# Kernel optimization log

Measured on AMD Instinct MI355X. Metric: run time of the kernel, lower is better.

Reference implementation:

```python
import jax, jax.numpy as jnp
import numpy as np

C = jnp.complex64
NQ = 4  # qubits per register (module-level `qubits` constant)

_CNOT = jnp.array([[1,0,0,0],[0,1,0,0],[0,0,0,1],[0,0,1,0]], dtype=C)
_X = jnp.array([[0,1],[1,0]], dtype=C)

def _RZ(t):
    e = jnp.exp((-0.5j) * t.astype(C))
    z = jnp.zeros((), C)
    return jnp.stack([jnp.stack([e, z]), jnp.stack([z, jnp.conj(e)])])

def _RX(t):
    c = jnp.cos(0.5 * t).astype(C)
    s = (-1j) * jnp.sin(0.5 * t).astype(C)
    return jnp.stack([jnp.stack([c, s]), jnp.stack([s, c])])

def _CRX(t):
    return jnp.eye(4, dtype=C).at[2:, 2:].set(_RX(t))

def _IXX(t):
    c = jnp.cos(0.5 * t).astype(C)
    s = (-1j) * jnp.sin(0.5 * t).astype(C)
    return c * jnp.eye(4, dtype=C) + s * jnp.fliplr(jnp.eye(4, dtype=C))

def _ap1(psi, U, w):
    psi = jnp.moveaxis(psi, w, 0)
    psi = jnp.tensordot(U, psi, axes=([1], [0]))
    return jnp.moveaxis(psi, 0, w)

def _ap2(psi, U, w1, w2):
    psi = jnp.moveaxis(psi, (w1, w2), (0, 1))
    shp = psi.shape
    psi = (U @ psi.reshape(4, -1)).reshape(shp)
    return jnp.moveaxis(psi, (0, 1), (w1, w2))

def _expZ(psi, w):
    p = psi.real ** 2 + psi.imag ** 2
    p = jnp.moveaxis(p, w, 0).reshape(2, -1).sum(axis=1)
    return p[0] - p[1]

def _expX(psi, w):
    return jnp.real(jnp.vdot(psi, _ap1(psi, _X, w)))

def _init_state(n):
    return jnp.zeros((2,) * n, C).at[(0,) * n].set(1.0 + 0.0j)

def _rot_layer(psi, rot, offset, start):
    for i in range(NQ):
        idx = start + 3 * i
        w = offset + i
        psi = _ap1(psi, _RZ(rot[idx]), w)
        psi = _ap1(psi, _RX(rot[idx + 1]), w)
        psi = _ap1(psi, _RZ(rot[idx + 2]), w)
    return psi

def _two_ring(psi, rot, crx, offset):
    # depth == 2 (24 rot params): one rot layer before entanglers, one after.
    psi = _rot_layer(psi, rot, offset, 0)
    for i in range(NQ):
        psi = _ap2(psi, _CRX(crx[i]), offset + i, offset + (i + 1) % NQ)
    for i in range(NQ):  # len(crx)==2*NQ -> IsingXX ring
        psi = _ap2(psi, _IXX(crx[NQ + i]), offset + i, offset + (i + 1) % NQ)
    psi = _rot_layer(psi, rot, offset, 3 * NQ)
    return psi

def _score_circuit(xq, xk, wq_rot, wq_crx, wk_rot, wk_crx, wc_rot, wc_crx, wc_crx2):
    psi = _init_state(2 * NQ)
    for i in range(NQ):  # AngleEmbedding (default rotation='X')
        psi = _ap1(psi, _RX(xq[i]), i)
    psi = _two_ring(psi, wq_rot, wq_crx, 0)
    for i in range(NQ):
        psi = _ap1(psi, _RX(xk[i]), NQ + i)
    psi = _two_ring(psi, wk_rot, wk_crx, NQ)
    for i in range(NQ):
        psi = _ap2(psi, _CRX(wc_crx[i]), i, i + NQ)
        psi = _ap2(psi, _CRX(wc_crx[i + NQ]), i + NQ, i)
    for i in range(NQ):
        psi = _ap2(psi, _CRX(wc_crx2[i]), i, (i + 1) % NQ + NQ)
    for i in range(NQ):
        psi = _ap2(psi, _CRX(wc_crx2[i + NQ]), i + NQ, (i + 1) % NQ)
    for i in range(NQ):
        psi = _ap2(psi, _CNOT, i, i + NQ)
        psi = _ap2(psi, _CNOT, i + NQ, i)
    psi = _rot_layer(psi, wc_rot, 0, 0)
    z = jnp.stack([_expZ(psi, w) for w in range(NQ)])
    x = jnp.stack([_expX(psi, w) for w in range(NQ)])
    return jnp.concatenate([z, x])

def _value_circuit(xv, amp, wv_rot, wv_crx, gates):
    psi = _init_state(NQ)
    for i in range(NQ):
        psi = _ap1(psi, _RX(xv[i]), i)
    psi = _two_ring(psi, wv_rot, wv_crx, 0)
    for i in range(NQ):
        psi = _ap1(psi, _RX(jnp.tanh(amp[i]) * gates[i]), i)
    for i in range(NQ):
        psi = _ap2(psi, _CNOT, i, (i + 1) % NQ)
    z = jnp.stack([_expZ(psi, w) for w in range(NQ)])
    x = jnp.stack([_expX(psi, w) for w in range(NQ)])
    return jnp.concatenate([z, x])

def setup_inputs() -> dict:
    key = jax.random.key(0)
    ks = jax.random.split(key, 16)
    B, IN = 4096, 96
    hp = np.pi / 2
    return {
        'x_text': jax.random.normal(ks[0], (B, IN), jnp.float32),
        'x_image': jax.random.normal(ks[1], (B, IN), jnp.float32),
        'W_text': jax.random.normal(ks[2], (NQ, IN), jnp.float32) * 0.1,
        'b_text': jnp.zeros((NQ,), jnp.float32),
        'W_image': jax.random.normal(ks[3], (NQ, IN), jnp.float32) * 0.1,
        'b_image': jnp.zeros((NQ,), jnp.float32),
        'weights_q_rot': jax.random.uniform(ks[4], (6 * NQ,), jnp.float32, -hp, hp),
        'weights_q_crx': jax.random.normal(ks[5], (2 * NQ,), jnp.float32) * 0.1,
        'weights_k_rot': jax.random.uniform(ks[6], (6 * NQ,), jnp.float32, -hp, hp),
        'weights_k_crx': jax.random.normal(ks[7], (2 * NQ,), jnp.float32) * 0.1,
        'weights_v_rot': jax.random.uniform(ks[8], (6 * NQ,), jnp.float32, -hp, hp),
        'weights_v_crx': jax.random.normal(ks[9], (2 * NQ,), jnp.float32) * 0.1,
        'weights_cross_rot': jax.random.uniform(ks[10], (3 * NQ,), jnp.float32, -hp, hp),
        'weights_cross_crx': jax.random.normal(ks[11], (2 * NQ,), jnp.float32) * 0.1,
        'weights_cross_crx2': jax.random.normal(ks[12], (2 * NQ,), jnp.float32) * 0.1,
        'score_gates': jnp.full((NQ,), np.pi, jnp.float32),
    }

def reference(x_text, x_image, W_text, b_text, W_image, b_image,
              weights_q_rot, weights_q_crx, weights_k_rot, weights_k_crx,
              weights_v_rot, weights_v_crx, weights_cross_rot,
              weights_cross_crx, weights_cross_crx2, score_gates):
    # anneal alpha = 1.0 and all QAFConfig flags True -> effective params = raw params
    xq = x_text @ W_text.T + b_text   # [B, 4]
    xk = x_image @ W_image.T + b_image
    score = jax.vmap(lambda a, b: _score_circuit(
        a, b, weights_q_rot, weights_q_crx, weights_k_rot, weights_k_crx,
        weights_cross_rot, weights_cross_crx, weights_cross_crx2))(xq, xk)  # [B, 8]
    amp = jnp.sqrt(score[:, :NQ] ** 2 + score[:, NQ:] ** 2)  # [B, 4]
    out = jax.vmap(lambda v, a: _value_circuit(
        v, a, weights_v_rot, weights_v_crx, score_gates))(xk, amp)  # [B, 8]
    return out.astype(jnp.float32)
```

## Files before the change

kernel.cpp:

```cpp
#include <hip/hip_runtime.h>
#include <math.h>

#define DEV __device__ __forceinline__

template<int M>
DEV float lxor(float x) {
    const int i = __builtin_bit_cast(int, x);
    int r;
    if constexpr (M == 1)      r = __builtin_amdgcn_update_dpp(i, i, 0xB1, 0xF, 0xF, false);
    else if constexpr (M == 2) r = __builtin_amdgcn_update_dpp(i, i, 0x4E, 0xF, 0xF, false);
    else if constexpr (M == 3) r = __builtin_amdgcn_update_dpp(i, i, 0x1B, 0xF, 0xF, false);
    else if constexpr (M == 8) r = __builtin_amdgcn_update_dpp(i, i, 0x128, 0xF, 0xF, false);
    else                       r = __builtin_amdgcn_ds_swizzle(i, (M << 10) | 0x1F);
    return __builtin_bit_cast(float, r);
}
template<int M> DEV float2 lxor2(float2 v) {
    return make_float2(lxor<M>(v.x), lxor<M>(v.y));
}
DEV float red16(float x) {
    x += lxor<8>(x); x += lxor<4>(x); x += lxor<2>(x); x += lxor<1>(x);
    return x;
}
DEV float red32(float x) {
    x += lxor<16>(x);
    return red16(x);
}

template<int LM>
DEV void sgate(float2& v, int l16, float2 u00, float2 u01) {
    const bool hi = (l16 & LM) != 0;
    const float e00x = u00.x, e00y = hi ? -u00.y : u00.y;
    const float e01x = hi ? -u01.x : u01.x, e01y = u01.y;
    const float2 p = lxor2<LM>(v);
    v = make_float2(e00x*v.x - e00y*v.y + e01x*p.x - e01y*p.y,
                    e00x*v.y + e00y*v.x + e01x*p.y + e01y*p.x);
}
template<int LM>
DEV void sgate4(float2& v, int l16, float4 g) {
    sgate<LM>(v, l16, make_float2(g.x, g.y), make_float2(g.z, g.w));
}
template<int CL, int LM>
DEV void scrx(float2& v, int l16, float2 cs) {
    const bool hi = (l16 & CL) != 0;
    const float c = hi ? cs.x : 1.f, sn = hi ? cs.y : 0.f;
    const float2 p = lxor2<LM>(v);
    v = make_float2(c*v.x + sn*p.y, c*v.y - sn*p.x);
}
template<int LM2>
DEV void sixx(float2& v, float2 cs) {
    const float2 p = lxor2<LM2>(v);
    v = make_float2(cs.x*v.x + cs.y*p.y, cs.x*v.y - cs.y*p.x);
}
template<int LM>
DEV void srx(float2& v, float c, float sn) {
    const float2 p = lxor2<LM>(v);
    v = make_float2(c*v.x + sn*p.y, c*v.y - sn*p.x);
}
template<int CL, int LM>
DEV void scnot(float2& v, int l16) {
    const float2 p = lxor2<LM>(v);
    const bool hi = (l16 & CL) != 0;
    v = hi ? p : v;
}

template<int CM, int LM>
DEV void fcrx_rl(float2 (&s)[8], float2 cs) {
#pragma unroll
    for (int r = 0; r < 8; r++) {
        if (!(r & CM)) continue;
        const float2 p = lxor2<LM>(s[r]);
        const float2 a = s[r];
        s[r] = make_float2(cs.x*a.x + cs.y*p.y, cs.x*a.y - cs.y*p.x);
    }
}
template<int CL, int RM>
DEV void fcrx_lr(float2 (&s)[8], int l32, float2 cs) {
    const bool hi = (l32 & CL) != 0;
    const float c = hi ? cs.x : 1.f, sn = hi ? cs.y : 0.f;
#pragma unroll
    for (int r = 0; r < 8; r++) {
        if (r & RM) continue;
        const int r1 = r | RM;
        const float2 a = s[r], b = s[r1];
        s[r]  = make_float2(c*a.x + sn*b.y, c*a.y - sn*b.x);
        s[r1] = make_float2(c*b.x + sn*a.y, c*b.y - sn*a.x);
    }
}
template<int CL, int LM>
DEV void fcrx_ll(float2 (&s)[8], int l32, float2 cs) {
    const bool hi = (l32 & CL) != 0;
    const float c = hi ? cs.x : 1.f, sn = hi ? cs.y : 0.f;
#pragma unroll
    for (int r = 0; r < 8; r++) {
        const float2 p = lxor2<LM>(s[r]);
        const float2 a = s[r];
        s[r] = make_float2(c*a.x + sn*p.y, c*a.y - sn*p.x);
    }
}
template<int CM, int LM>
DEV void fcnot_rl(float2 (&s)[8]) {
#pragma unroll
    for (int r = 0; r < 8; r++)
        if (r & CM) s[r] = lxor2<LM>(s[r]);
}
template<int CL, int RM>
DEV void fcnot_lr(float2 (&s)[8], int l32) {
    const bool hi = (l32 & CL) != 0;
#pragma unroll
    for (int r = 0; r < 8; r++) {
        if (r & RM) continue;
        const int r1 = r | RM;
        const float2 a = s[r], b = s[r1];
        s[r]  = hi ? b : a;
        s[r1] = hi ? a : b;
    }
}
template<int CL, int LM>
DEV void fcnot_ll(float2 (&s)[8], int l32) {
    const bool hi = (l32 & CL) != 0;
#pragma unroll
    for (int r = 0; r < 8; r++) {
        const float2 p = lxor2<LM>(s[r]);
        s[r] = hi ? p : s[r];
    }
}

template<int RM>
DEV void measR(const float2 (&s)[8], const float (&n2)[8],
               float4 mz, float2 bx, float& z, float& x) {
    float zz = 0.f, xx = 0.f;
#pragma unroll
    for (int r = 0; r < 8; r++) {
        if (r & RM) continue;
        const int r1 = r | RM;
        const float nd  = n2[r] - n2[r1];
        const float dre = s[r].x*s[r1].x + s[r].y*s[r1].y;
        const float dim = s[r].x*s[r1].y - s[r].y*s[r1].x;
        zz += mz.x*nd + mz.y*dre - mz.z*dim;
        xx += mz.w*nd + bx.x*dre - bx.y*dim;
    }
    z = zz; x = xx;
}
DEV void measL16(const float2 (&s)[8], const float (&n2)[8], int l32,
                 float4 mz, float2 bx, float& z, float& x) {
    const float f = (l32 & 16) ? -1.f : 1.f;
    float zz = 0.f, xx = 0.f;
#pragma unroll
    for (int r = 0; r < 8; r++) {
        const float2 p = lxor2<16>(s[r]);
        const float tre = s[r].x*p.x + s[r].y*p.y;
        const float ftim = f * (s[r].x*p.y - s[r].y*p.x);
        const float fn = f * n2[r];
        zz += mz.x*fn + 0.5f*(mz.y*tre - mz.z*ftim);
        xx += mz.w*fn + 0.5f*(bx.x*tre - bx.y*ftim);
    }
    z = zz; x = xx;
}

DEV void fuse_rx(float4 g, float ang, float2& u00, float2& u01) {
    float s_, c_;
    __sincosf(0.5f * ang, &s_, &c_);
    u00 = make_float2(g.x*c_ + g.w*s_, g.y*c_ - g.z*s_);
    u01 = make_float2(g.y*s_ + g.z*c_, -g.x*s_ + g.w*c_);
}

__global__ __launch_bounds__(256, 2) void qa_kernel(
    const float* __restrict__ x_text, const float* __restrict__ x_image,
    const float* __restrict__ W_text, const float* __restrict__ b_text,
    const float* __restrict__ W_image, const float* __restrict__ b_image,
    const float* __restrict__ wq_rot, const float* __restrict__ wq_crx,
    const float* __restrict__ wk_rot, const float* __restrict__ wk_crx,
    const float* __restrict__ wv_rot, const float* __restrict__ wv_crx,
    const float* __restrict__ wc_rot, const float* __restrict__ wc_crx,
    const float* __restrict__ wc_crx2, const float* __restrict__ gates,
    float* __restrict__ out, int B)
{
    __shared__ float4 sG[28];
    __shared__ float2 sCS[40];
    __shared__ float4 sWT[192];
    __shared__ float4 sMZ[4];
    __shared__ float2 sBX[4];
    __shared__ __align__(16) float2 sQK[8][32];

    const int tid = threadIdx.x;
    if (tid < 192) {
        const float* W = (tid < 96) ? W_text : W_image;
        const int idx = (tid < 96) ? tid : tid - 96;
        sWT[tid] = make_float4(W[idx], W[96 + idx], W[192 + idx], W[288 + idx]);
    }
    if (tid < 28) {
        const float* srcs[7] = {wq_rot, wq_rot + 12, wk_rot, wk_rot + 12,
                                wc_rot, wv_rot, wv_rot + 12};
        const float* p = srcs[tid >> 2] + 3 * (tid & 3);
        const float a = p[0], bb = p[1], c = p[2];
        float sh, ch, sd, cd, sb, cb;
        __sincosf(0.5f * (a + c), &sh, &ch);
        __sincosf(0.5f * (a - c), &sd, &cd);
        __sincosf(0.5f * bb, &sb, &cb);
        const float4 g = make_float4(cb * ch, -cb * sh, sb * sd, -sb * cd);
        sG[tid] = g;
        if (tid >= 16 && tid < 20) {
            const int w = tid - 16;
            const float2 u00 = make_float2(g.x, g.y), u01 = make_float2(g.z, g.w);
            const float az = u00.x*u00.x + u00.y*u00.y - u01.x*u01.x - u01.y*u01.y;
            sMZ[w] = make_float4(az,
                                 4.f*(u00.x*u01.x + u00.y*u01.y),
                                 4.f*(u00.x*u01.y - u00.y*u01.x),
                                 -2.f*(u00.x*u01.x - u00.y*u01.y));
            sBX[w] = make_float2(
                2.f*(u00.x*u00.x - u00.y*u00.y - u01.x*u01.x + u01.y*u01.y),
                -4.f*(u00.x*u00.y + u01.x*u01.y));
        }
    }
    if (tid < 40) {
        const float* srcs[5] = {wq_crx, wk_crx, wc_crx, wc_crx2, wv_crx};
        const float t = srcs[tid >> 3][tid & 7];
        float s_, c_;
        __sincosf(0.5f * t, &s_, &c_);
        sCS[tid] = make_float2(c_, s_);
    }
    __syncthreads();

    const int l32 = tid & 31;
    const int l16 = tid & 15;
    const int hi = (l32 >> 4) & 1;
    const int elem = tid >> 5;
    const int b = blockIdx.x * 8 + elem;

    const float* xt = x_text + (size_t)b * 96;
    const float* xi = x_image + (size_t)b * 96;
    float aq[4] = {0.f, 0.f, 0.f, 0.f}, ak[4] = {0.f, 0.f, 0.f, 0.f};
#pragma unroll
    for (int kk = 0; kk < 3; kk++) {
        const int idx = l32 + 32 * kk;
        const float vq = xt[idx], vk = xi[idx];
        const float4 wq = sWT[idx], wk = sWT[96 + idx];
        aq[0] += vq * wq.x; aq[1] += vq * wq.y; aq[2] += vq * wq.z; aq[3] += vq * wq.w;
        ak[0] += vk * wk.x; ak[1] += vk * wk.y; ak[2] += vk * wk.z; ak[3] += vk * wk.w;
    }
    float xq[4], xk[4];
#pragma unroll
    for (int j = 0; j < 4; j++) {
        xq[j] = red32(aq[j]) + b_text[j];
        xk[j] = red32(ak[j]) + b_image[j];
    }

    const float4* gA = sG + (hi ? 8 : 0);
    const float2* cA = sCS + (hi ? 8 : 0);
    float2 A = make_float2((l16 == 0) ? 1.f : 0.f, 0.f);
    float2 V = A;
    {
        float2 u00, u01;
        fuse_rx(gA[0], hi ? xk[0] : xq[0], u00, u01); sgate<8>(A, l16, u00, u01);
        fuse_rx(sG[20], xk[0], u00, u01);             sgate<8>(V, l16, u00, u01);
        fuse_rx(gA[1], hi ? xk[1] : xq[1], u00, u01); sgate<4>(A, l16, u00, u01);
        fuse_rx(sG[21], xk[1], u00, u01);             sgate<4>(V, l16, u00, u01);
        fuse_rx(gA[2], hi ? xk[2] : xq[2], u00, u01); sgate<2>(A, l16, u00, u01);
        fuse_rx(sG[22], xk[2], u00, u01);             sgate<2>(V, l16, u00, u01);
        fuse_rx(gA[3], hi ? xk[3] : xq[3], u00, u01); sgate<1>(A, l16, u00, u01);
        fuse_rx(sG[23], xk[3], u00, u01);             sgate<1>(V, l16, u00, u01);
    }
    scrx<8, 4>(A, l16, cA[0]);  scrx<8, 4>(V, l16, sCS[32]);
    scrx<4, 2>(A, l16, cA[1]);  scrx<4, 2>(V, l16, sCS[33]);
    scrx<2, 1>(A, l16, cA[2]);  scrx<2, 1>(V, l16, sCS[34]);
    scrx<1, 8>(A, l16, cA[3]);  scrx<1, 8>(V, l16, sCS[35]);
    sixx<12>(A, cA[4]);  sixx<12>(V, sCS[36]);
    sixx<6>(A, cA[5]);   sixx<6>(V, sCS[37]);
    sixx<3>(A, cA[6]);   sixx<3>(V, sCS[38]);
    sixx<9>(A, cA[7]);   sixx<9>(V, sCS[39]);
    sgate4<8>(A, l16, gA[4]);  sgate4<8>(V, l16, sG[24]);
    sgate4<4>(A, l16, gA[5]);  sgate4<4>(V, l16, sG[25]);
    sgate4<2>(A, l16, gA[6]);  sgate4<2>(V, l16, sG[26]);
    sgate4<1>(A, l16, gA[7]);  sgate4<1>(V, l16, sG[27]);

    sQK[elem][(hi << 4) | l16] = A;
    asm volatile("" ::: "memory");
    const float2 kk2 = sQK[elem][16 + l16];
    const float4* qrow = reinterpret_cast<const float4*>(&sQK[elem][hi << 3]);
    float2 s[8];
#pragma unroll
    for (int j = 0; j < 4; j++) {
        const float4 t = qrow[j];
        s[2*j]   = make_float2(t.x*kk2.x - t.y*kk2.y, t.x*kk2.y + t.y*kk2.x);
        s[2*j+1] = make_float2(t.z*kk2.x - t.w*kk2.y, t.z*kk2.y + t.w*kk2.x);
    }

    fcrx_ll<16, 8>(s, l32, sCS[16]); fcrx_ll<8, 16>(s, l32, sCS[20]);
    fcrx_rl<4, 4>(s, sCS[17]);       fcrx_lr<4, 4>(s, l32, sCS[21]);
    fcrx_rl<2, 2>(s, sCS[18]);       fcrx_lr<2, 2>(s, l32, sCS[22]);
    fcrx_rl<1, 1>(s, sCS[19]);       fcrx_lr<1, 1>(s, l32, sCS[23]);
    fcrx_ll<16, 4>(s, l32, sCS[24]);
    fcrx_rl<4, 2>(s, sCS[25]);
    fcrx_rl<2, 1>(s, sCS[26]);
    fcrx_rl<1, 8>(s, sCS[27]);
    fcrx_lr<8, 4>(s, l32, sCS[28]);
    fcrx_lr<4, 2>(s, l32, sCS[29]);
    fcrx_lr<2, 1>(s, l32, sCS[30]);
    fcrx_ll<1, 16>(s, l32, sCS[31]);
    fcnot_ll<16, 8>(s, l32); fcnot_ll<8, 16>(s, l32);
    fcnot_rl<4, 4>(s);       fcnot_lr<4, 4>(s, l32);
    fcnot_rl<2, 2>(s);       fcnot_lr<2, 2>(s, l32);
    fcnot_rl<1, 1>(s);       fcnot_lr<1, 1>(s, l32);

    float n2[8];
#pragma unroll
    for (int r = 0; r < 8; r++) n2[r] = s[r].x*s[r].x + s[r].y*s[r].y;
    float amp[4];
    {
        float z0, x0, z1, x1, z2, x2, z3, x3;
        measL16(s, n2, l32, sMZ[0], sBX[0], z0, x0);
        measR<4>(s, n2, sMZ[1], sBX[1], z1, x1);
        measR<2>(s, n2, sMZ[2], sBX[2], z2, x2);
        measR<1>(s, n2, sMZ[3], sBX[3], z3, x3);
        z0 = red32(z0); x0 = red32(x0);
        z1 = red32(z1); x1 = red32(x1);
        z2 = red32(z2); x2 = red32(x2);
        z3 = red32(z3); x3 = red32(x3);
        amp[0] = sqrtf(z0*z0 + x0*x0);
        amp[1] = sqrtf(z1*z1 + x1*x1);
        amp[2] = sqrtf(z2*z2 + x2*x2);
        amp[3] = sqrtf(z3*z3 + x3*x3);
    }

#pragma unroll
    for (int i = 0; i < 4; i++) {
        const float e = __expf(2.f * amp[i]);
        const float th = 1.f - 2.f / (e + 1.f);
        const float ang = th * gates[i];
        float s_, c_;
        __sincosf(0.5f * ang, &s_, &c_);
        if (i == 0) srx<8>(V, c_, s_);
        if (i == 1) srx<4>(V, c_, s_);
        if (i == 2) srx<2>(V, c_, s_);
        if (i == 3) srx<1>(V, c_, s_);
    }
    scnot<8, 4>(V, l16); scnot<4, 2>(V, l16);
    scnot<2, 1>(V, l16); scnot<1, 8>(V, l16);

    const float vn2 = V.x*V.x + V.y*V.y;
    float oz[4], ox[4];
    {
        const float2 p8 = lxor2<8>(V), p4 = lxor2<4>(V),
                     p2 = lxor2<2>(V), p1 = lxor2<1>(V);
        oz[0] = red16((l16 & 8) ? -vn2 : vn2);
        oz[1] = red16((l16 & 4) ? -vn2 : vn2);
        oz[2] = red16((l16 & 2) ? -vn2 : vn2);
        oz[3] = red16((l16 & 1) ? -vn2 : vn2);
        ox[0] = red16(V.x*p8.x + V.y*p8.y);
        ox[1] = red16(V.x*p4.x + V.y*p4.y);
        ox[2] = red16(V.x*p2.x + V.y*p2.y);
        ox[3] = red16(V.x*p1.x + V.y*p1.y);
    }
    if (l32 == 0) {
        float4* o = (float4*)(out + (size_t)b * 8);
        o[0] = make_float4(oz[0], oz[1], oz[2], oz[3]);
        o[1] = make_float4(ox[0], ox[1], ox[2], ox[3]);
    }
}

extern "C" void kernel_launch(void* const* d_in, const int* in_sizes, int n_in,
                              void* d_out, int out_size, void* d_ws, size_t ws_size,
                              hipStream_t stream) {
    (void)n_in; (void)out_size; (void)d_ws; (void)ws_size;
    const int B = in_sizes[0] / 96;
    const dim3 grid((B + 7) / 8), block(256);
    hipLaunchKernelGGL(qa_kernel, grid, block, 0, stream,
                       (const float*)d_in[0], (const float*)d_in[1],
                       (const float*)d_in[2], (const float*)d_in[3],
                       (const float*)d_in[4], (const float*)d_in[5],
                       (const float*)d_in[6], (const float*)d_in[7],
                       (const float*)d_in[8], (const float*)d_in[9],
                       (const float*)d_in[10], (const float*)d_in[11],
                       (const float*)d_in[12], (const float*)d_in[13],
                       (const float*)d_in[14], (const float*)d_in[15],
                       (float*)d_out, B);
}
```

Before: 94.37 us.

## Map each batch element to a full 64-lane wavefront with 4 amplitudes per lane

Each batch element now gets a 64-lane wave instead of 32 lanes. The four 16-lane groups separately evolve the q, k, cross and value registers, replacing the interleaved A/V evolution. The 256-amplitude joint state is split 4 per lane, and gates across the 32-lane boundary use ds_bpermute. The final CNOT ring is a single permutation plus swaps, and the launch-bounds occupancy hint rises from 2 to 4. This halves per-lane register work and serial gate chains, but doubles the lanes used per element and adds slower bpermute LDS-path shuffles.

```diff
diff --git a/kernel.cpp b/kernel.cpp
--- a/kernel.cpp
+++ b/kernel.cpp
@@ -17,6 +17,13 @@
 template<int M> DEV float2 lxor2(float2 v) {
     return make_float2(lxor<M>(v.x), lxor<M>(v.y));
 }
+DEV float bpermf(int addr, float x) {
+    return __builtin_bit_cast(float,
+        __builtin_amdgcn_ds_bpermute(addr, __builtin_bit_cast(int, x)));
+}
+DEV float2 bperm2(int addr, float2 v) {
+    return make_float2(bpermf(addr, v.x), bpermf(addr, v.y));
+}
 DEV float red16(float x) {
     x += lxor<8>(x); x += lxor<4>(x); x += lxor<2>(x); x += lxor<1>(x);
     return x;
@@ -24,6 +31,10 @@
 DEV float red32(float x) {
     x += lxor<16>(x);
     return red16(x);
+}
+DEV float red64(float x, int a32) {
+    x += bpermf(a32, x);
+    return red32(x);
 }
 
 template<int LM>
@@ -63,22 +74,54 @@
     v = hi ? p : v;
 }
 
+template<int CL, int LM>
+DEV void xcrx_ll(float2 (&s)[4], int ln, float2 cs) {
+    const bool hi = (ln & CL) != 0;
+    const float c = hi ? cs.x : 1.f, sn = hi ? cs.y : 0.f;
+#pragma unroll
+    for (int r = 0; r < 4; r++) {
+        const float2 p = lxor2<LM>(s[r]);
+        const float2 a = s[r];
+        s[r] = make_float2(c*a.x + sn*p.y, c*a.y - sn*p.x);
+    }
+}
+template<int CL>
+DEV void xcrx_l32(float2 (&s)[4], int ln, int a32, float2 cs) {
+    const bool hi = (ln & CL) != 0;
+    const float c = hi ? cs.x : 1.f, sn = hi ? cs.y : 0.f;
+#pragma unroll
+    for (int r = 0; r < 4; r++) {
+        const float2 p = bperm2(a32, s[r]);
+        const float2 a = s[r];
+        s[r] = make_float2(c*a.x + sn*p.y, c*a.y - sn*p.x);
+    }
+}
 template<int CM, int LM>
-DEV void fcrx_rl(float2 (&s)[8], float2 cs) {
-#pragma unroll
-    for (int r = 0; r < 8; r++) {
+DEV void xcrx_rl(float2 (&s)[4], float2 cs) {
+#pragma unroll
+    for (int r = 0; r < 4; r++) {
         if (!(r & CM)) continue;
         const float2 p = lxor2<LM>(s[r]);
         const float2 a = s[r];
         s[r] = make_float2(cs.x*a.x + cs.y*p.y, cs.x*a.y - cs.y*p.x);
     }
 }
+template<int CM>
+DEV void xcrx_r32(float2 (&s)[4], int a32, float2 cs) {
+#pragma unroll
+    for (int r = 0; r < 4; r++) {
+        if (!(r & CM)) continue;
+        const float2 p = bperm2(a32, s[r]);
+        const float2 a = s[r];
+        s[r] = make_float2(cs.x*a.x + cs.y*p.y, cs.x*a.y - cs.y*p.x);
+    }
+}
 template<int CL, int RM>
-DEV void fcrx_lr(float2 (&s)[8], int l32, float2 cs) {
-    const bool hi = (l32 & CL) != 0;
+DEV void xcrx_lr(float2 (&s)[4], int ln, float2 cs) {
+    const bool hi = (ln & CL) != 0;
     const float c = hi ? cs.x : 1.f, sn = hi ? cs.y : 0.f;
 #pragma unroll
-    for (int r = 0; r < 8; r++) {
+    for (int r = 0; r < 4; r++) {
         if (r & RM) continue;
         const int r1 = r | RM;
         const float2 a = s[r], b = s[r1];
@@ -86,51 +129,13 @@
         s[r1] = make_float2(c*b.x + sn*a.y, c*b.y - sn*a.x);
     }
 }
-template<int CL, int LM>
-DEV void fcrx_ll(float2 (&s)[8], int l32, float2 cs) {
-    const bool hi = (l32 & CL) != 0;
-    const float c = hi ? cs.x : 1.f, sn = hi ? cs.y : 0.f;
-#pragma unroll
-    for (int r = 0; r < 8; r++) {
-        const float2 p = lxor2<LM>(s[r]);
-        const float2 a = s[r];
-        s[r] = make_float2(c*a.x + sn*p.y, c*a.y - sn*p.x);
-    }
-}
-template<int CM, int LM>
-DEV void fcnot_rl(float2 (&s)[8]) {
-#pragma unroll
-    for (int r = 0; r < 8; r++)
-        if (r & CM) s[r] = lxor2<LM>(s[r]);
-}
-template<int CL, int RM>
-DEV void fcnot_lr(float2 (&s)[8], int l32) {
-    const bool hi = (l32 & CL) != 0;
-#pragma unroll
-    for (int r = 0; r < 8; r++) {
-        if (r & RM) continue;
-        const int r1 = r | RM;
-        const float2 a = s[r], b = s[r1];
-        s[r]  = hi ? b : a;
-        s[r1] = hi ? a : b;
-    }
-}
-template<int CL, int LM>
-DEV void fcnot_ll(float2 (&s)[8], int l32) {
-    const bool hi = (l32 & CL) != 0;
-#pragma unroll
-    for (int r = 0; r < 8; r++) {
-        const float2 p = lxor2<LM>(s[r]);
-        s[r] = hi ? p : s[r];
-    }
-}
 
 template<int RM>
-DEV void measR(const float2 (&s)[8], const float (&n2)[8],
-               float4 mz, float2 bx, float& z, float& x) {
+DEV void measRR(const float2 (&s)[4], const float (&n2)[4],
+                float4 mz, float2 bx, float& z, float& x) {
     float zz = 0.f, xx = 0.f;
 #pragma unroll
-    for (int r = 0; r < 8; r++) {
+    for (int r = 0; r < 4; r++) {
         if (r & RM) continue;
         const int r1 = r | RM;
         const float nd  = n2[r] - n2[r1];
@@ -141,13 +146,14 @@
     }
     z = zz; x = xx;
 }
-DEV void measL16(const float2 (&s)[8], const float (&n2)[8], int l32,
-                 float4 mz, float2 bx, float& z, float& x) {
-    const float f = (l32 & 16) ? -1.f : 1.f;
+template<int LM>
+DEV void measLn(const float2 (&s)[4], const float (&n2)[4], int ln,
+                float4 mz, float2 bx, float& z, float& x) {
+    const float f = (ln & LM) ? -1.f : 1.f;
     float zz = 0.f, xx = 0.f;
 #pragma unroll
-    for (int r = 0; r < 8; r++) {
-        const float2 p = lxor2<16>(s[r]);
+    for (int r = 0; r < 4; r++) {
+        const float2 p = lxor2<LM>(s[r]);
         const float tre = s[r].x*p.x + s[r].y*p.y;
         const float ftim = f * (s[r].x*p.y - s[r].y*p.x);
         const float fn = f * n2[r];
@@ -164,7 +170,7 @@
     u01 = make_float2(g.y*s_ + g.z*c_, -g.x*s_ + g.w*c_);
 }
 
-__global__ __launch_bounds__(256, 2) void qa_kernel(
+__global__ __launch_bounds__(256, 4) void qa_kernel(
     const float* __restrict__ x_text, const float* __restrict__ x_image,
     const float* __restrict__ W_text, const float* __restrict__ b_text,
     const float* __restrict__ W_image, const float* __restrict__ b_image,
@@ -180,7 +186,8 @@
     __shared__ float4 sWT[192];
     __shared__ float4 sMZ[4];
     __shared__ float2 sBX[4];
-    __shared__ __align__(16) float2 sQK[8][32];
+    __shared__ float  sB[8];
+    __shared__ __align__(16) float2 sQK[4][32];
 
     const int tid = threadIdx.x;
     if (tid < 192) {
@@ -219,103 +226,122 @@
         __sincosf(0.5f * t, &s_, &c_);
         sCS[tid] = make_float2(c_, s_);
     }
+    if (tid < 8) sB[tid] = (tid < 4) ? b_text[tid] : b_image[tid - 4];
     __syncthreads();
 
-    const int l32 = tid & 31;
-    const int l16 = tid & 15;
-    const int hi = (l32 >> 4) & 1;
-    const int elem = tid >> 5;
-    const int b = blockIdx.x * 8 + elem;
-
-    const float* xt = x_text + (size_t)b * 96;
-    const float* xi = x_image + (size_t)b * 96;
-    float aq[4] = {0.f, 0.f, 0.f, 0.f}, ak[4] = {0.f, 0.f, 0.f, 0.f};
+    const int ln   = tid & 63;
+    const int l16  = ln & 15;
+    const int l32  = ln & 31;
+    const int half = ln >> 5;
+    const int g    = ln >> 4;
+    const int elem = tid >> 6;
+    const int b    = blockIdx.x * 4 + elem;
+    if (b >= B) return;
+
+    const float* xsrc = (half ? x_image : x_text) + (size_t)b * 96;
+    const float4* wbase = sWT + 96 * half;
+    float acc[4] = {0.f, 0.f, 0.f, 0.f};
 #pragma unroll
     for (int kk = 0; kk < 3; kk++) {
         const int idx = l32 + 32 * kk;
-        const float vq = xt[idx], vk = xi[idx];
-        const float4 wq = sWT[idx], wk = sWT[96 + idx];
-        aq[0] += vq * wq.x; aq[1] += vq * wq.y; aq[2] += vq * wq.z; aq[3] += vq * wq.w;
-        ak[0] += vk * wk.x; ak[1] += vk * wk.y; ak[2] += vk * wk.z; ak[3] += vk * wk.w;
-    }
-    float xq[4], xk[4];
-#pragma unroll
-    for (int j = 0; j < 4; j++) {
-        xq[j] = red32(aq[j]) + b_text[j];
-        xk[j] = red32(ak[j]) + b_image[j];
-    }
-
-    const float4* gA = sG + (hi ? 8 : 0);
-    const float2* cA = sCS + (hi ? 8 : 0);
+        const float v = xsrc[idx];
+        const float4 w = wbase[idx];
+        acc[0] += v * w.x; acc[1] += v * w.y; acc[2] += v * w.z; acc[3] += v * w.w;
+    }
+    float xv[4];
+#pragma unroll
+    for (int j = 0; j < 4; j++) xv[j] = red32(acc[j]) + sB[4 * half + j];
+
+    const int gb = (g < 2) ? 0 : (g == 2 ? 8 : 20);
+    const int cb = (g < 2) ? 0 : (g == 2 ? 8 : 32);
     float2 A = make_float2((l16 == 0) ? 1.f : 0.f, 0.f);
-    float2 V = A;
     {
         float2 u00, u01;
-        fuse_rx(gA[0], hi ? xk[0] : xq[0], u00, u01); sgate<8>(A, l16, u00, u01);
-        fuse_rx(sG[20], xk[0], u00, u01);             sgate<8>(V, l16, u00, u01);
-        fuse_rx(gA[1], hi ? xk[1] : xq[1], u00, u01); sgate<4>(A, l16, u00, u01);
-        fuse_rx(sG[21], xk[1], u00, u01);             sgate<4>(V, l16, u00, u01);
-        fuse_rx(gA[2], hi ? xk[2] : xq[2], u00, u01); sgate<2>(A, l16, u00, u01);
-        fuse_rx(sG[22], xk[2], u00, u01);             sgate<2>(V, l16, u00, u01);
-        fuse_rx(gA[3], hi ? xk[3] : xq[3], u00, u01); sgate<1>(A, l16, u00, u01);
-        fuse_rx(sG[23], xk[3], u00, u01);             sgate<1>(V, l16, u00, u01);
-    }
-    scrx<8, 4>(A, l16, cA[0]);  scrx<8, 4>(V, l16, sCS[32]);
-    scrx<4, 2>(A, l16, cA[1]);  scrx<4, 2>(V, l16, sCS[33]);
-    scrx<2, 1>(A, l16, cA[2]);  scrx<2, 1>(V, l16, sCS[34]);
-    scrx<1, 8>(A, l16, cA[3]);  scrx<1, 8>(V, l16, sCS[35]);
-    sixx<12>(A, cA[4]);  sixx<12>(V, sCS[36]);
-    sixx<6>(A, cA[5]);   sixx<6>(V, sCS[37]);
-    sixx<3>(A, cA[6]);   sixx<3>(V, sCS[38]);
-    sixx<9>(A, cA[7]);   sixx<9>(V, sCS[39]);
-    sgate4<8>(A, l16, gA[4]);  sgate4<8>(V, l16, sG[24]);
-    sgate4<4>(A, l16, gA[5]);  sgate4<4>(V, l16, sG[25]);
-    sgate4<2>(A, l16, gA[6]);  sgate4<2>(V, l16, sG[26]);
-    sgate4<1>(A, l16, gA[7]);  sgate4<1>(V, l16, sG[27]);
-
-    sQK[elem][(hi << 4) | l16] = A;
+        fuse_rx(sG[gb + 0], xv[0], u00, u01); sgate<8>(A, l16, u00, u01);
+        fuse_rx(sG[gb + 1], xv[1], u00, u01); sgate<4>(A, l16, u00, u01);
+        fuse_rx(sG[gb + 2], xv[2], u00, u01); sgate<2>(A, l16, u00, u01);
+        fuse_rx(sG[gb + 3], xv[3], u00, u01); sgate<1>(A, l16, u00, u01);
+    }
+    scrx<8, 4>(A, l16, sCS[cb + 0]);
+    scrx<4, 2>(A, l16, sCS[cb + 1]);
+    scrx<2, 1>(A, l16, sCS[cb + 2]);
+    scrx<1, 8>(A, l16, sCS[cb + 3]);
+    sixx<12>(A, sCS[cb + 4]);
+    sixx<6>(A, sCS[cb + 5]);
+    sixx<3>(A, sCS[cb + 6]);
+    sixx<9>(A, sCS[cb + 7]);
+    sgate4<8>(A, l16, sG[gb + 4]);
+    sgate4<4>(A, l16, sG[gb + 5]);
+    sgate4<2>(A, l16, sG[gb + 6]);
+    sgate4<1>(A, l16, sG[gb + 7]);
+
+    if (!(g & 1)) sQK[elem][(g ? 16 : 0) + l16] = A;
     asm volatile("" ::: "memory");
-    const float2 kk2 = sQK[elem][16 + l16];
-    const float4* qrow = reinterpret_cast<const float4*>(&sQK[elem][hi << 3]);
-    float2 s[8];
-#pragma unroll
-    for (int j = 0; j < 4; j++) {
-        const float4 t = qrow[j];
-        s[2*j]   = make_float2(t.x*kk2.x - t.y*kk2.y, t.x*kk2.y + t.y*kk2.x);
-        s[2*j+1] = make_float2(t.z*kk2.x - t.w*kk2.y, t.z*kk2.y + t.w*kk2.x);
-    }
-
-    fcrx_ll<16, 8>(s, l32, sCS[16]); fcrx_ll<8, 16>(s, l32, sCS[20]);
-    fcrx_rl<4, 4>(s, sCS[17]);       fcrx_lr<4, 4>(s, l32, sCS[21]);
-    fcrx_rl<2, 2>(s, sCS[18]);       fcrx_lr<2, 2>(s, l32, sCS[22]);
-    fcrx_rl<1, 1>(s, sCS[19]);       fcrx_lr<1, 1>(s, l32, sCS[23]);
-    fcrx_ll<16, 4>(s, l32, sCS[24]);
-    fcrx_rl<4, 2>(s, sCS[25]);
-    fcrx_rl<2, 1>(s, sCS[26]);
-    fcrx_rl<1, 8>(s, sCS[27]);
-    fcrx_lr<8, 4>(s, l32, sCS[28]);
-    fcrx_lr<4, 2>(s, l32, sCS[29]);
-    fcrx_lr<2, 1>(s, l32, sCS[30]);
-    fcrx_ll<1, 16>(s, l32, sCS[31]);
-    fcnot_ll<16, 8>(s, l32); fcnot_ll<8, 16>(s, l32);
-    fcnot_rl<4, 4>(s);       fcnot_lr<4, 4>(s, l32);
-    fcnot_rl<2, 2>(s);       fcnot_lr<2, 2>(s, l32);
-    fcnot_rl<1, 1>(s);       fcnot_lr<1, 1>(s, l32);
-
-    float n2[8];
-#pragma unroll
-    for (int r = 0; r < 8; r++) n2[r] = s[r].x*s[r].x + s[r].y*s[r].y;
+    const int kidx = ((ln >> 5) & 1) * 8 + (ln & 7);
+    const int qb   = ((ln >> 4) & 1) * 8 + ((ln >> 3) & 1) * 4;
+    const float2 kk2 = sQK[elem][16 + kidx];
+    const float4* qrow = reinterpret_cast<const float4*>(&sQK[elem][qb]);
+    float2 s[4];
+    {
+        const float4 t0 = qrow[0], t1 = qrow[1];
+        s[0] = make_float2(t0.x*kk2.x - t0.y*kk2.y, t0.x*kk2.y + t0.y*kk2.x);
+        s[1] = make_float2(t0.z*kk2.x - t0.w*kk2.y, t0.z*kk2.y + t0.w*kk2.x);
+        s[2] = make_float2(t1.x*kk2.x - t1.y*kk2.y, t1.x*kk2.y + t1.y*kk2.x);
+        s[3] = make_float2(t1.z*kk2.x - t1.w*kk2.y, t1.z*kk2.y + t1.w*kk2.x);
+    }
+
+    const int a32 = (ln ^ 32) << 2;
+    xcrx_l32<16>(s, ln, a32, sCS[16]);
+    xcrx_ll<32, 16>(s, ln, sCS[20]);
+    xcrx_ll<8, 4>(s, ln, sCS[17]);
+    xcrx_ll<4, 8>(s, ln, sCS[21]);
+    xcrx_rl<2, 2>(s, sCS[18]);
+    xcrx_lr<2, 2>(s, ln, sCS[22]);
+    xcrx_rl<1, 1>(s, sCS[19]);
+    xcrx_lr<1, 1>(s, ln, sCS[23]);
+    xcrx_ll<16, 4>(s, ln, sCS[24]);
+    xcrx_ll<8, 2>(s, ln, sCS[25]);
+    xcrx_rl<2, 1>(s, sCS[26]);
+    xcrx_r32<1>(s, a32, sCS[27]);
+    xcrx_ll<32, 8>(s, ln, sCS[28]);
+    xcrx_lr<4, 2>(s, ln, sCS[29]);
+    xcrx_lr<2, 1>(s, ln, sCS[30]);
+    xcrx_ll<1, 16>(s, ln, sCS[31]);
+    {
+        const int b5 = (ln >> 5) & 1, b4 = (ln >> 4) & 1;
+        const int b3 = (ln >> 3) & 1, b2 = (ln >> 2) & 1;
+        const int aperm = ((b4 << 5) | ((b4 ^ b5) << 4) | ((b3 ^ b2) << 3) |
+                          (b3 << 2) | (ln & 3)) << 2;
+#pragma unroll
+        for (int r = 0; r < 4; r++) s[r] = bperm2(aperm, s[r]);
+    }
+    s[2] = lxor2<2>(s[2]); s[3] = lxor2<2>(s[3]);
+    {
+        const bool hi = (ln & 2) != 0;
+        const float2 a0 = s[0], a2 = s[2]; s[0] = hi ? a2 : a0; s[2] = hi ? a0 : a2;
+        const float2 a1 = s[1], a3 = s[3]; s[1] = hi ? a3 : a1; s[3] = hi ? a1 : a3;
+    }
+    s[1] = lxor2<1>(s[1]); s[3] = lxor2<1>(s[3]);
+    {
+        const bool hi = (ln & 1) != 0;
+        const float2 a0 = s[0], a1 = s[1]; s[0] = hi ? a1 : a0; s[1] = hi ? a0 : a1;
+        const float2 a2 = s[2], a3 = s[3]; s[2] = hi ? a3 : a2; s[3] = hi ? a2 : a3;
+    }
+
+    float n2[4];
+#pragma unroll
+    for (int r = 0; r < 4; r++) n2[r] = s[r].x*s[r].x + s[r].y*s[r].y;
     float amp[4];
     {
         float z0, x0, z1, x1, z2, x2, z3, x3;
-        measL16(s, n2, l32, sMZ[0], sBX[0], z0, x0);
-        measR<4>(s, n2, sMZ[1], sBX[1], z1, x1);
-        measR<2>(s, n2, sMZ[2], sBX[2], z2, x2);
-        measR<1>(s, n2, sMZ[3], sBX[3], z3, x3);
-        z0 = red32(z0); x0 = red32(x0);
-        z1 = red32(z1); x1 = red32(x1);
-        z2 = red32(z2); x2 = red32(x2);
-        z3 = red32(z3); x3 = red32(x3);
+        measLn<16>(s, n2, ln, sMZ[0], sBX[0], z0, x0);
+        measLn<8>(s, n2, ln, sMZ[1], sBX[1], z1, x1);
+        measRR<2>(s, n2, sMZ[2], sBX[2], z2, x2);
+        measRR<1>(s, n2, sMZ[3], sBX[3], z3, x3);
+        z0 = red64(z0, a32); x0 = red64(x0, a32);
+        z1 = red64(z1, a32); x1 = red64(x1, a32);
+        z2 = red64(z2, a32); x2 = red64(x2, a32);
+        z3 = red64(z3, a32); x3 = red64(x3, a32);
         amp[0] = sqrtf(z0*z0 + x0*x0);
         amp[1] = sqrtf(z1*z1 + x1*x1);
         amp[2] = sqrtf(z2*z2 + x2*x2);
@@ -329,29 +355,29 @@
         const float ang = th * gates[i];
         float s_, c_;
         __sincosf(0.5f * ang, &s_, &c_);
-        if (i == 0) srx<8>(V, c_, s_);
-        if (i == 1) srx<4>(V, c_, s_);
-        if (i == 2) srx<2>(V, c_, s_);
-        if (i == 3) srx<1>(V, c_, s_);
-    }
-    scnot<8, 4>(V, l16); scnot<4, 2>(V, l16);
-    scnot<2, 1>(V, l16); scnot<1, 8>(V, l16);
-
-    const float vn2 = V.x*V.x + V.y*V.y;
+        if (i == 0) srx<8>(A, c_, s_);
+        if (i == 1) srx<4>(A, c_, s_);
+        if (i == 2) srx<2>(A, c_, s_);
+        if (i == 3) srx<1>(A, c_, s_);
+    }
+    scnot<8, 4>(A, l16); scnot<4, 2>(A, l16);
+    scnot<2, 1>(A, l16); scnot<1, 8>(A, l16);
+
+    const float vn2 = A.x*A.x + A.y*A.y;
     float oz[4], ox[4];
     {
-        const float2 p8 = lxor2<8>(V), p4 = lxor2<4>(V),
-                     p2 = lxor2<2>(V), p1 = lxor2<1>(V);
+        const float2 p8 = lxor2<8>(A), p4 = lxor2<4>(A),
+                     p2 = lxor2<2>(A), p1 = lxor2<1>(A);
         oz[0] = red16((l16 & 8) ? -vn2 : vn2);
         oz[1] = red16((l16 & 4) ? -vn2 : vn2);
         oz[2] = red16((l16 & 2) ? -vn2 : vn2);
         oz[3] = red16((l16 & 1) ? -vn2 : vn2);
-        ox[0] = red16(V.x*p8.x + V.y*p8.y);
-        ox[1] = red16(V.x*p4.x + V.y*p4.y);
-        ox[2] = red16(V.x*p2.x + V.y*p2.y);
-        ox[3] = red16(V.x*p1.x + V.y*p1.y);
-    }
-    if (l32 == 0) {
+        ox[0] = red16(A.x*p8.x + A.y*p8.y);
+        ox[1] = red16(A.x*p4.x + A.y*p4.y);
+        ox[2] = red16(A.x*p2.x + A.y*p2.y);
+        ox[3] = red16(A.x*p1.x + A.y*p1.y);
+    }
+    if (ln == 48) {
         float4* o = (float4*)(out + (size_t)b * 8);
         o[0] = make_float4(oz[0], oz[1], oz[2], oz[3]);
         o[1] = make_float4(ox[0], ox[1], ox[2], ox[3]);
@@ -363,7 +389,7 @@
                               hipStream_t stream) {
     (void)n_in; (void)out_size; (void)d_ws; (void)ws_size;
     const int B = in_sizes[0] / 96;
-    const dim3 grid((B + 7) / 8), block(256);
+    const dim3 grid((B + 3) / 4), block(256);
     hipLaunchKernelGGL(qa_kernel, grid, block, 0, stream,
                        (const float*)d_in[0], (const float*)d_in[1],
                        (const float*)d_in[2], (const float*)d_in[3],
```

Result: no change. 93.98 us (-0.4%).
